# Optimization experiments

Measured on AMD Instinct MI355X. Metric: run time of the kernel, lower is better.

## Reference

```python
import jax, jax.numpy as jnp
import numpy as np

B, N, E, H = 4, 2048, 256, 8
D = E // H
EPS = 1e-5


def _layernorm(x, g, b):
    mu = jnp.mean(x, axis=-1, keepdims=True)
    var = jnp.mean(jnp.square(x - mu), axis=-1, keepdims=True)
    return (x - mu) * jax.lax.rsqrt(var + EPS) * g + b


def setup_inputs() -> dict:
    key = jax.random.key(0)
    ks = jax.random.split(key, 8)
    s = 1.0 / np.sqrt(E)
    lin = lambda k: (jax.random.normal(k, (E, E), jnp.float32) * s)
    return {
        "x_l": jax.random.normal(ks[0], (B, N, E), jnp.float32),
        "x_r": jax.random.normal(ks[1], (B, N, E), jnp.float32),
        "Wq": lin(ks[2]), "bq": jnp.zeros((E,), jnp.float32),
        "Wk": lin(ks[3]), "bk": jnp.zeros((E,), jnp.float32),
        "Wv": lin(ks[4]), "bv": jnp.zeros((E,), jnp.float32),
        "Wp": lin(ks[5]), "bp": jnp.zeros((E,), jnp.float32),
        "ln_g": jnp.ones((E,), jnp.float32), "ln_b": jnp.zeros((E,), jnp.float32),
        "rn_g": jnp.ones((E,), jnp.float32), "rn_b": jnp.zeros((E,), jnp.float32),
    }


def reference(x_l, x_r, Wq, bq, Wk, bk, Wv, bv, Wp, bp, ln_g, ln_b, rn_g, rn_b):
    # projections -> [b, h, n, d]
    q = (x_l @ Wq + bq).reshape(B, N, H, D).transpose(0, 2, 1, 3)
    k = (x_r @ Wk + bk).reshape(B, N, H, D).transpose(0, 2, 1, 3)
    # shared value from the difference of the two streams
    v = ((x_l - x_r) @ Wv + bv).reshape(B, N, H, D).transpose(0, 2, 1, 3)

    energy = jnp.einsum('bhqd,bhkd->bhqk', q, k)  # [b,h,n,n]
    attn = jax.nn.softmax(energy / np.sqrt(D), axis=-1)  # dropout p=0 (eval)

    # attn used as-is and transposed against the SAME value tensor
    out_l = jnp.einsum('bhqk,bhkd->bhqd', attn, v)
    out_r = jnp.einsum('bhqk,bhqd->bhkd', attn, v)  # == attn^T @ v

    out_l = out_l.transpose(0, 2, 1, 3).reshape(B, N, E)
    out_r = out_r.transpose(0, 2, 1, 3).reshape(B, N, E)

    out_l = _layernorm(out_l @ Wp + bp, ln_g, ln_b) + x_l
    out_r = _layernorm(out_r @ Wp + bp, rn_g, rn_b) + x_r
    return (out_l, out_r)
```

## Files before the change

### kernel.cpp

```cpp
#include <hip/hip_runtime.h>
#include <math.h>


typedef __attribute__((ext_vector_type(8))) short short8;
typedef __attribute__((ext_vector_type(4))) float f32x4;
typedef __attribute__((ext_vector_type(16))) float f32x16;
typedef __attribute__((ext_vector_type(4))) unsigned short u16x4;

union FragU { unsigned int u[4]; short8 s8; };

__device__ __forceinline__ unsigned short bf16_rn(float f) {
    union { float f; unsigned int u; } c; c.f = f;
    return (unsigned short)((c.u + 0x7FFFu + ((c.u >> 16) & 1u)) >> 16);
}
__device__ __forceinline__ float b2f(unsigned short u) {
    union { unsigned int i; float f; } c; c.i = ((unsigned int)u) << 16;
    return c.f;
}

#if __has_builtin(__builtin_amdgcn_exp2f)
__device__ __forceinline__ float fexp2(float x) { return __builtin_amdgcn_exp2f(x); }
#else
__device__ __forceinline__ float fexp2(float x) { return exp2f(x); }
#endif

__device__ __forceinline__ f32x4 mfma16(short8 a, short8 b, f32x4 c) {
    return __builtin_amdgcn_mfma_f32_16x16x32_bf16(a, b, c, 0, 0, 0);
}
__device__ __forceinline__ f32x16 mfma32(short8 a, short8 b, f32x16 c) {
    return __builtin_amdgcn_mfma_f32_32x32x16_bf16(a, b, c, 0, 0, 0);
}

__device__ __forceinline__ void plswap(unsigned int& x, unsigned int& y) {
    asm("v_permlane32_swap_b32 %0, %1" : "+v"(x), "+v"(y));
}

__device__ __forceinline__ short8 pfrag(unsigned int w0, unsigned int w1,
                                        unsigned int w2, unsigned int w3) {
    plswap(w0, w2);
    plswap(w1, w3);
    FragU fu;
    fu.u[0] = w0; fu.u[1] = w1; fu.u[2] = w2; fu.u[3] = w3;
    return fu.s8;
}

__global__ void prep_x(const float* __restrict__ xl, const float* __restrict__ xr,
                       unsigned short* __restrict__ xlb, unsigned short* __restrict__ xrb,
                       unsigned short* __restrict__ xdb) {
    const size_t i = ((size_t)blockIdx.x * 256 + threadIdx.x) * 4;
    const float4 A = *(const float4*)(xl + i);
    const float4 Bv = *(const float4*)(xr + i);
    u16x4 pa = { bf16_rn(A.x), bf16_rn(A.y), bf16_rn(A.z), bf16_rn(A.w) };
    u16x4 pb = { bf16_rn(Bv.x), bf16_rn(Bv.y), bf16_rn(Bv.z), bf16_rn(Bv.w) };
    u16x4 pd = { bf16_rn(A.x - Bv.x), bf16_rn(A.y - Bv.y),
                 bf16_rn(A.z - Bv.z), bf16_rn(A.w - Bv.w) };
    *(u16x4*)(xlb + i) = pa;
    *(u16x4*)(xrb + i) = pb;
    *(u16x4*)(xdb + i) = pd;
}

__global__ void prep_w(const float* __restrict__ Wq, const float* __restrict__ Wk,
                       const float* __restrict__ Wv, const float* __restrict__ Wp,
                       unsigned short* __restrict__ Wqt, unsigned short* __restrict__ Wkt,
                       unsigned short* __restrict__ Wvt, unsigned short* __restrict__ Wpt) {
    const int gid = blockIdx.x * 256 + threadIdx.x;
    const int m = gid >> 16;
    const int idx = gid & 65535;
    const int k = idx >> 8, n = idx & 255;
    const float* W = (m == 0) ? Wq : (m == 1) ? Wk : (m == 2) ? Wv : Wp;
    unsigned short* Wt = (m == 0) ? Wqt : (m == 1) ? Wkt : (m == 2) ? Wvt : Wpt;
    Wt[n * 256 + k] = bf16_rn(W[(size_t)k * 256 + n]);
}

__launch_bounds__(256)
__global__ void qkv_gemm(const unsigned short* __restrict__ xlb,
                         const unsigned short* __restrict__ xrb,
                         const unsigned short* __restrict__ xdb,
                         const unsigned short* __restrict__ Wqt,
                         const unsigned short* __restrict__ Wkt,
                         const unsigned short* __restrict__ Wvt,
                         const float* __restrict__ bq, const float* __restrict__ bk,
                         const float* __restrict__ bv,
                         unsigned short* __restrict__ Qg, unsigned short* __restrict__ Kg,
                         unsigned short* __restrict__ Vtg) {
    const int z = blockIdx.z;
    const unsigned short* A  = (z == 0) ? xlb : (z == 1) ? xrb : xdb;
    const unsigned short* Wt = (z == 0) ? Wqt : (z == 1) ? Wkt : Wvt;
    const float* bias        = (z == 0) ? bq  : (z == 1) ? bk  : bv;

    __shared__ unsigned short At[128][40];
    __shared__ unsigned short Bt[64][40];

    const int tid = threadIdx.x;
    const int lane = tid & 63, wv = tid >> 6;
    const int a = lane & 15, g = lane >> 4;
    const int wr = wv >> 1, wc = wv & 1;
    const int r0 = blockIdx.x * 128;
    const int c0 = blockIdx.y * 64;

    const f32x4 fz = {0.f, 0.f, 0.f, 0.f};
    f32x4 acc[4][2];
#pragma unroll
    for (int f = 0; f < 4; ++f)
#pragma unroll
        for (int t = 0; t < 2; ++t) acc[f][t] = fz;

    const int arow = tid >> 1, aoff = (tid & 1) * 16;
    const int brow = tid >> 2, boff = (tid & 3) * 8;

    for (int ks = 0; ks < 8; ++ks) {
        __syncthreads();
        {
            const unsigned short* asrc = A + (size_t)(r0 + arow) * 256 + ks * 32 + aoff;
            *(short8*)&At[arow][aoff]     = *(const short8*)asrc;
            *(short8*)&At[arow][aoff + 8] = *(const short8*)(asrc + 8);
            *(short8*)&Bt[brow][boff] =
                *(const short8*)(Wt + (size_t)(c0 + brow) * 256 + ks * 32 + boff);
        }
        __syncthreads();
        short8 af[4], bfr[2];
#pragma unroll
        for (int f = 0; f < 4; ++f) af[f] = *(const short8*)&At[wr * 64 + f * 16 + a][g * 8];
#pragma unroll
        for (int t = 0; t < 2; ++t) bfr[t] = *(const short8*)&Bt[wc * 32 + t * 16 + a][g * 8];
#pragma unroll
        for (int f = 0; f < 4; ++f)
#pragma unroll
            for (int t = 0; t < 2; ++t) acc[f][t] = mfma16(af[f], bfr[t], acc[f][t]);
    }

    const float scq = 0.17677669529663687f * 1.4426950408889634f;
#pragma unroll
    for (int t = 0; t < 2; ++t) {
        const int C = c0 + wc * 32 + t * 16 + a;
        const float bb = bias[C];
        const int h = C >> 5, d = C & 31;
#pragma unroll
        for (int f = 0; f < 4; ++f) {
            const int Rb = r0 + wr * 64 + f * 16 + g * 4;
            const int b_ = Rb >> 11, n = Rb & 2047;
            const int bhh = b_ * 8 + h;
            float v[4];
#pragma unroll
            for (int r = 0; r < 4; ++r) {
                v[r] = acc[f][t][r] + bb;
                if (z == 0) v[r] *= scq;
            }
            if (z < 2) {
                unsigned short* dst = ((z == 0) ? Qg : Kg) + (size_t)(bhh * 2048 + n) * 32 + d;
#pragma unroll
                for (int r = 0; r < 4; ++r) dst[(size_t)r * 32] = bf16_rn(v[r]);
            } else {
                u16x4 pk = { bf16_rn(v[0]), bf16_rn(v[1]), bf16_rn(v[2]), bf16_rn(v[3]) };
                *(u16x4*)(Vtg + (size_t)(bhh * 32 + d) * 2048 + n) = pk;
            }
        }
    }
}

#define P1_STEP(T, CUR)                                                         \
    {                                                                           \
        if ((T) < 31) *(short8*)((CUR) ? sd0 : sd1) = rr;                       \
        if ((T) < 30) rr = *(const short8*)(sgb + (size_t)(z * 32 + (T) + 2) * gstep); \
        const unsigned short* sb = (CUR) ? stz1 : stz0;                         \
        const short8 ck0 = *(const short8*)(sb + ro);                           \
        const short8 ck1 = *(const short8*)(sb + 512 + ro);                     \
        const short8 cv0 = *(const short8*)(sb + 1024 + ro);                    \
        const short8 cv1 = *(const short8*)(sb + 1536 + ro);                    \
        f32x16 s = {};                                                          \
        s = mfma32(ck0, qf0, s);                                                \
        s = mfma32(ck1, qf1, s);                                                \
        float p[16];                                                            \
        _Pragma("unroll") for (int j = 0; j < 16; ++j) p[j] = fexp2(s[j]);      \
        l_run += ((p[0] + p[1]) + (p[2] + p[3])) + ((p[4] + p[5]) + (p[6] + p[7])) \
               + ((p[8] + p[9]) + (p[10] + p[11])) + ((p[12] + p[13]) + (p[14] + p[15])); \
        unsigned int w[8];                                                      \
        _Pragma("unroll") for (int mm = 0; mm < 8; ++mm)                        \
            asm("v_cvt_pk_bf16_f32 %0, %1, %2"                                  \
                : "=v"(w[mm]) : "v"(p[2 * mm]), "v"(p[2 * mm + 1]));            \
        acc = mfma32(cv0, pfrag(w[0], w[1], w[2], w[3]), acc);                  \
        acc = mfma32(cv1, pfrag(w[4], w[5], w[6], w[7]), acc);                  \
        __syncthreads();                                                        \
    }

__launch_bounds__(512, 4)
__global__ void attn_pass1(const unsigned short* __restrict__ Qg,
                           const unsigned short* __restrict__ Kg,
                           const unsigned short* __restrict__ Vtg,
                           unsigned short* __restrict__ AOl,
                           unsigned short* __restrict__ Vsg) {
    __shared__ unsigned short ST[2][2][2][2][64][8];
    __shared__ float accS[4][16][64];
    __shared__ float lsumS[4][64];

    const int f = blockIdx.x;
    const int bh = 4 * (f & 7) + (f >> 7);
    const int qblk = (f >> 3) & 15;
    const int tid = threadIdx.x;
    const int wv = tid >> 6;
    const int qi = wv & 3, z = wv >> 2;
    const int lane = tid & 63, l31 = lane & 31, hi = lane >> 5;
    const int q0 = qblk * 128 + qi * 32;

    const unsigned short* Qb = Qg + (size_t)bh * 2048 * 32;
    const unsigned short* Kb = Kg + (size_t)bh * 2048 * 32;
    const unsigned short* Vb = Vtg + (size_t)bh * 32 * 2048;

    const short8 qf0 = *(const short8*)(Qb + (size_t)(q0 + l31) * 32 + hi * 8);
    const short8 qf1 = *(const short8*)(Qb + (size_t)(q0 + l31) * 32 + 16 + hi * 8);

    const int kv = qi >> 1;
    const int srow = (qi & 1) * 16 + (lane >> 2);
    const int m = lane & 3;
    unsigned short* sd0 = &ST[z][0][kv][m >> 1][srow + 32 * (m & 1)][0];
    unsigned short* sd1 = &ST[z][1][kv][m >> 1][srow + 32 * (m & 1)][0];
    const size_t gstep = kv ? 32 : 1024;
    const unsigned short* sgb = kv
        ? Vb + (size_t)srow * 2048 + m * 8
        : Kb + (size_t)srow * 32 + m * 8;

    const unsigned short* stz0 = &ST[z][0][0][0][0][0];
    const unsigned short* stz1 = &ST[z][1][0][0][0][0];
    const int ro = (l31 + 32 * hi) * 8;

    f32x16 acc = {};
    float l_run = 0.f;

    short8 rr = *(const short8*)(sgb + (size_t)(z * 32) * gstep);
    *(short8*)sd0 = rr;
    rr = *(const short8*)(sgb + (size_t)(z * 32 + 1) * gstep);
    __syncthreads();

    for (int tt = 0; tt < 16; ++tt) {
        P1_STEP(2 * tt, 0)
        P1_STEP(2 * tt + 1, 1)
    }

    float lsum = l_run + __shfl_xor(l_run, 32);

    if (z == 1) {
#pragma unroll
        for (int j = 0; j < 16; ++j) accS[qi][j][lane] = acc[j];
        lsumS[qi][lane] = lsum;
    }
    __syncthreads();
    if (z == 0) {
        lsum += lsumS[qi][lane];
        const float rl = 1.0f / lsum;
#pragma unroll
        for (int j = 0; j < 16; ++j) acc[j] += accS[qi][j][lane];

        const int b_ = bh >> 3, h = bh & 7;
        const int q = q0 + l31;
        unsigned short* dst = AOl + (size_t)(b_ * 2048 + q) * 256 + h * 32;
#pragma unroll
        for (int g2 = 0; g2 < 4; ++g2) {
            u16x4 pk = { bf16_rn(acc[4 * g2 + 0] * rl), bf16_rn(acc[4 * g2 + 1] * rl),
                         bf16_rn(acc[4 * g2 + 2] * rl), bf16_rn(acc[4 * g2 + 3] * rl) };
            *(u16x4*)(dst + 8 * g2 + 4 * hi) = pk;
        }
        if (hi == 0) lsumS[qi][l31] = rl;
    }
    __syncthreads();
    if (z == 1) {
        const int cb = hi * 16;
        float il[16];
#pragma unroll
        for (int e = 0; e < 16; e += 4) {
            const float4 v4 = *(const float4*)&lsumS[qi][cb + e];
            il[e] = v4.x; il[e + 1] = v4.y; il[e + 2] = v4.z; il[e + 3] = v4.w;
        }
        const unsigned short* vsrc = Vb + (size_t)l31 * 2048 + q0 + cb;
        unsigned short* vdst = Vsg + (size_t)bh * 32 * 2048 + (size_t)l31 * 2048 + q0 + cb;
#pragma unroll
        for (int c4 = 0; c4 < 4; ++c4) {
            const u16x4 vv = *(const u16x4*)(vsrc + c4 * 4);
            u16x4 o = { bf16_rn(b2f(vv.x) * il[c4 * 4 + 0]),
                        bf16_rn(b2f(vv.y) * il[c4 * 4 + 1]),
                        bf16_rn(b2f(vv.z) * il[c4 * 4 + 2]),
                        bf16_rn(b2f(vv.w) * il[c4 * 4 + 3]) };
            *(u16x4*)(vdst + c4 * 4) = o;
        }
    }
}

#define P2_STEP(T, CUR)                                                         \
    {                                                                           \
        if ((T) < 31) *(short8*)((CUR) ? sd0 : sd1) = rr;                       \
        if ((T) < 30) rr = *(const short8*)(sgb + (size_t)(z * 32 + (T) + 2) * gstep); \
        const unsigned short* sb = (CUR) ? stz1 : stz0;                         \
        const short8 cq0 = *(const short8*)(sb + ro);                           \
        const short8 cq1 = *(const short8*)(sb + 512 + ro);                     \
        const short8 cv0 = *(const short8*)(sb + 1024 + ro);                    \
        const short8 cv1 = *(const short8*)(sb + 1536 + ro);                    \
        f32x16 s = {};                                                          \
        s = mfma32(cq0, kf0, s);                                                \
        s = mfma32(cq1, kf1, s);                                                \
        float p[16];                                                            \
        _Pragma("unroll") for (int j = 0; j < 16; ++j) p[j] = fexp2(s[j]);      \
        unsigned int w[8];                                                      \
        _Pragma("unroll") for (int mm = 0; mm < 8; ++mm)                        \
            asm("v_cvt_pk_bf16_f32 %0, %1, %2"                                  \
                : "=v"(w[mm]) : "v"(p[2 * mm]), "v"(p[2 * mm + 1]));            \
        acc = mfma32(pfrag(w[0], w[1], w[2], w[3]), cv0, acc);                  \
        acc = mfma32(pfrag(w[4], w[5], w[6], w[7]), cv1, acc);                  \
        __syncthreads();                                                        \
    }

__launch_bounds__(512, 4)
__global__ void attn_pass2(const unsigned short* __restrict__ Qg,
                           const unsigned short* __restrict__ Kg,
                           const unsigned short* __restrict__ Vsg,
                           unsigned short* __restrict__ AOr) {
    __shared__ unsigned short ST[2][2][2][2][64][8];
    __shared__ float accS[4][16][64];

    const int f = blockIdx.x;
    const int bh = 4 * (f & 7) + (f >> 7);
    const int kblk = (f >> 3) & 15;
    const int tid = threadIdx.x;
    const int wv = tid >> 6;
    const int ki = wv & 3, z = wv >> 2;
    const int lane = tid & 63, l31 = lane & 31, hi = lane >> 5;
    const int k0 = kblk * 128 + ki * 32;

    const unsigned short* Qb = Qg + (size_t)bh * 2048 * 32;
    const unsigned short* Kb = Kg + (size_t)bh * 2048 * 32;
    const unsigned short* Vb = Vsg + (size_t)bh * 32 * 2048;

    const short8 kf0 = *(const short8*)(Kb + (size_t)(k0 + l31) * 32 + hi * 8);
    const short8 kf1 = *(const short8*)(Kb + (size_t)(k0 + l31) * 32 + 16 + hi * 8);

    const int kv = ki >> 1;
    const int srow = (ki & 1) * 16 + (lane >> 2);
    const int m = lane & 3;
    unsigned short* sd0 = &ST[z][0][kv][m >> 1][srow + 32 * (m & 1)][0];
    unsigned short* sd1 = &ST[z][1][kv][m >> 1][srow + 32 * (m & 1)][0];
    const size_t gstep = kv ? 32 : 1024;
    const unsigned short* sgb = kv
        ? Vb + (size_t)srow * 2048 + m * 8
        : Qb + (size_t)srow * 32 + m * 8;

    const unsigned short* stz0 = &ST[z][0][0][0][0][0];
    const unsigned short* stz1 = &ST[z][1][0][0][0][0];
    const int ro = (l31 + 32 * hi) * 8;

    f32x16 acc = {};

    short8 rr = *(const short8*)(sgb + (size_t)(z * 32) * gstep);
    *(short8*)sd0 = rr;
    rr = *(const short8*)(sgb + (size_t)(z * 32 + 1) * gstep);
    __syncthreads();

    for (int tt = 0; tt < 16; ++tt) {
        P2_STEP(2 * tt, 0)
        P2_STEP(2 * tt + 1, 1)
    }

    if (z == 1) {
#pragma unroll
        for (int j = 0; j < 16; ++j) accS[ki][j][lane] = acc[j];
    }
    __syncthreads();
    if (z == 0) {
#pragma unroll
        for (int j = 0; j < 16; ++j) acc[j] += accS[ki][j][lane];

        const int b_ = bh >> 3, h = bh & 7;
#pragma unroll
        for (int j = 0; j < 16; ++j) {
            const int krow = k0 + (j & 3) + 8 * (j >> 2) + 4 * hi;
            AOr[(size_t)(b_ * 2048 + krow) * 256 + h * 32 + l31] = bf16_rn(acc[j]);
        }
    }
}

__launch_bounds__(256)
__global__ void proj_ln(const unsigned short* __restrict__ AO,
                        const unsigned short* __restrict__ Wpt,
                        const float* __restrict__ bp,
                        const float* __restrict__ gamma, const float* __restrict__ beta,
                        const float* __restrict__ xres,
                        float* __restrict__ out) {
    __shared__ unsigned short At[64][264];
    __shared__ unsigned short Bt[256][40];

    const int tid = threadIdx.x;
    const int lane = tid & 63, wv = tid >> 6;
    const int a = lane & 15, g = lane >> 4;
    const int r0 = blockIdx.x * 64;

    {
        const int row = tid >> 2, seg = (tid & 3) * 64;
        const unsigned short* src = AO + (size_t)(r0 + row) * 256 + seg;
#pragma unroll
        for (int i = 0; i < 8; ++i)
            *(short8*)&At[row][seg + i * 8] = *(const short8*)(src + i * 8);
    }

    const f32x4 fz = {0.f, 0.f, 0.f, 0.f};
    f32x4 acc[16];
#pragma unroll
    for (int cf = 0; cf < 16; ++cf) acc[cf] = fz;

    for (int ks = 0; ks < 8; ++ks) {
        __syncthreads();
        {
            const unsigned short* src = Wpt + (size_t)tid * 256 + ks * 32;
#pragma unroll
            for (int i = 0; i < 4; ++i)
                *(short8*)&Bt[tid][i * 8] = *(const short8*)(src + i * 8);
        }
        __syncthreads();
        const short8 af = *(const short8*)&At[wv * 16 + a][ks * 32 + g * 8];
#pragma unroll
        for (int cf = 0; cf < 16; ++cf) {
            const short8 bfr = *(const short8*)&Bt[cf * 16 + a][g * 8];
            acc[cf] = mfma16(af, bfr, acc[cf]);
        }
    }

    float bb[16], gg[16], be[16];
#pragma unroll
    for (int cf = 0; cf < 16; ++cf) {
        const int c = cf * 16 + a;
        bb[cf] = bp[c]; gg[cf] = gamma[c]; be[cf] = beta[c];
    }
#pragma unroll
    for (int r = 0; r < 4; ++r) {
        float y[16];
        float s1 = 0.f, s2 = 0.f;
#pragma unroll
        for (int cf = 0; cf < 16; ++cf) {
            y[cf] = acc[cf][r] + bb[cf];
            s1 += y[cf];
            s2 += y[cf] * y[cf];
        }
#pragma unroll
        for (int mask = 1; mask <= 8; mask <<= 1) {
            s1 += __shfl_xor(s1, mask);
            s2 += __shfl_xor(s2, mask);
        }
        const float mu = s1 * (1.0f / 256.0f);
        const float var = s2 * (1.0f / 256.0f) - mu * mu;
        const float rstd = rsqrtf(var + 1e-5f);
        const int R = r0 + wv * 16 + g * 4 + r;
#pragma unroll
        for (int cf = 0; cf < 16; ++cf) {
            const int c = cf * 16 + a;
            out[(size_t)R * 256 + c] =
                (y[cf] - mu) * rstd * gg[cf] + be[cf] + xres[(size_t)R * 256 + c];
        }
    }
}

extern "C" void kernel_launch(void* const* d_in, const int* in_sizes, int n_in,
                              void* d_out, int out_size, void* d_ws, size_t ws_size,
                              hipStream_t stream) {
    const float* x_l  = (const float*)d_in[0];
    const float* x_r  = (const float*)d_in[1];
    const float* Wq   = (const float*)d_in[2];
    const float* bq   = (const float*)d_in[3];
    const float* Wk   = (const float*)d_in[4];
    const float* bk   = (const float*)d_in[5];
    const float* Wv   = (const float*)d_in[6];
    const float* bv   = (const float*)d_in[7];
    const float* Wp   = (const float*)d_in[8];
    const float* bp   = (const float*)d_in[9];
    const float* ln_g = (const float*)d_in[10];
    const float* ln_b = (const float*)d_in[11];
    const float* rn_g = (const float*)d_in[12];
    const float* rn_b = (const float*)d_in[13];

    const size_t SZ_TOK = (size_t)8192 * 256;

    unsigned short* xl_bf = (unsigned short*)d_ws;
    unsigned short* xr_bf = xl_bf + SZ_TOK;
    unsigned short* xd_bf = xr_bf + SZ_TOK;
    unsigned short* Qg    = xd_bf + SZ_TOK;
    unsigned short* Kg    = Qg + SZ_TOK;
    unsigned short* Vtg   = Kg + SZ_TOK;
    unsigned short* Wqt   = Vtg + SZ_TOK;
    unsigned short* Wkt   = Wqt + 65536;
    unsigned short* Wvt   = Wkt + 65536;
    unsigned short* Wpt   = Wvt + 65536;
    unsigned short* AOl   = xl_bf;
    unsigned short* AOr   = xr_bf;
    unsigned short* Vs    = xd_bf;
    float* out = (float*)d_out;

    prep_x<<<2048, 256, 0, stream>>>(x_l, x_r, xl_bf, xr_bf, xd_bf);
    prep_w<<<1024, 256, 0, stream>>>(Wq, Wk, Wv, Wp, Wqt, Wkt, Wvt, Wpt);
    qkv_gemm<<<dim3(64, 4, 3), 256, 0, stream>>>(xl_bf, xr_bf, xd_bf,
                                                 Wqt, Wkt, Wvt, bq, bk, bv, Qg, Kg, Vtg);
    attn_pass1<<<512, 512, 0, stream>>>(Qg, Kg, Vtg, AOl, Vs);
    attn_pass2<<<512, 512, 0, stream>>>(Qg, Kg, Vs, AOr);
    proj_ln<<<128, 256, 0, stream>>>(AOl, Wpt, bp, ln_g, ln_b, x_l, out);
    proj_ln<<<128, 256, 0, stream>>>(AOr, Wpt, bp, rn_g, rn_b, x_r, out + SZ_TOK);
}
```

Baseline: 104.2 us.

## Double-buffer GEMM and attention tiles, merge prep and proj launches

Merges the prep_x and prep_w kernels into one launch, and the two proj_ln launches into one grid that uses blockIdx.y to pick the stream. Adds LDS double-buffering in qkv_gemm and proj_ln so the next K-slice is staged while the current one is consumed, leaving one barrier per step. The attention passes now stage two KV tiles per phase and sync once per pair instead of once per tile. The aim is fewer launches and less barrier stall, at the cost of more shared memory, which may lower occupancy in the 4-blocks-per-CU attention kernels.

Result: faster. 90.37 us (-13.3%).

```diff
diff --git a/kernel.cpp b/kernel.cpp
--- a/kernel.cpp
+++ b/kernel.cpp
@@ -44,32 +44,34 @@
     return fu.s8;
 }
 
-__global__ void prep_x(const float* __restrict__ xl, const float* __restrict__ xr,
-                       unsigned short* __restrict__ xlb, unsigned short* __restrict__ xrb,
-                       unsigned short* __restrict__ xdb) {
-    const size_t i = ((size_t)blockIdx.x * 256 + threadIdx.x) * 4;
-    const float4 A = *(const float4*)(xl + i);
-    const float4 Bv = *(const float4*)(xr + i);
-    u16x4 pa = { bf16_rn(A.x), bf16_rn(A.y), bf16_rn(A.z), bf16_rn(A.w) };
-    u16x4 pb = { bf16_rn(Bv.x), bf16_rn(Bv.y), bf16_rn(Bv.z), bf16_rn(Bv.w) };
-    u16x4 pd = { bf16_rn(A.x - Bv.x), bf16_rn(A.y - Bv.y),
-                 bf16_rn(A.z - Bv.z), bf16_rn(A.w - Bv.w) };
-    *(u16x4*)(xlb + i) = pa;
-    *(u16x4*)(xrb + i) = pb;
-    *(u16x4*)(xdb + i) = pd;
-}
-
-__global__ void prep_w(const float* __restrict__ Wq, const float* __restrict__ Wk,
-                       const float* __restrict__ Wv, const float* __restrict__ Wp,
-                       unsigned short* __restrict__ Wqt, unsigned short* __restrict__ Wkt,
-                       unsigned short* __restrict__ Wvt, unsigned short* __restrict__ Wpt) {
-    const int gid = blockIdx.x * 256 + threadIdx.x;
-    const int m = gid >> 16;
-    const int idx = gid & 65535;
-    const int k = idx >> 8, n = idx & 255;
-    const float* W = (m == 0) ? Wq : (m == 1) ? Wk : (m == 2) ? Wv : Wp;
-    unsigned short* Wt = (m == 0) ? Wqt : (m == 1) ? Wkt : (m == 2) ? Wvt : Wpt;
-    Wt[n * 256 + k] = bf16_rn(W[(size_t)k * 256 + n]);
+__global__ void prep_all(const float* __restrict__ xl, const float* __restrict__ xr,
+                         const float* __restrict__ Wq, const float* __restrict__ Wk,
+                         const float* __restrict__ Wv, const float* __restrict__ Wp,
+                         unsigned short* __restrict__ xlb, unsigned short* __restrict__ xrb,
+                         unsigned short* __restrict__ xdb,
+                         unsigned short* __restrict__ Wqt, unsigned short* __restrict__ Wkt,
+                         unsigned short* __restrict__ Wvt, unsigned short* __restrict__ Wpt) {
+    const int bid = blockIdx.x;
+    if (bid < 2048) {
+        const size_t i = ((size_t)bid * 256 + threadIdx.x) * 4;
+        const float4 A = *(const float4*)(xl + i);
+        const float4 Bv = *(const float4*)(xr + i);
+        u16x4 pa = { bf16_rn(A.x), bf16_rn(A.y), bf16_rn(A.z), bf16_rn(A.w) };
+        u16x4 pb = { bf16_rn(Bv.x), bf16_rn(Bv.y), bf16_rn(Bv.z), bf16_rn(Bv.w) };
+        u16x4 pd = { bf16_rn(A.x - Bv.x), bf16_rn(A.y - Bv.y),
+                     bf16_rn(A.z - Bv.z), bf16_rn(A.w - Bv.w) };
+        *(u16x4*)(xlb + i) = pa;
+        *(u16x4*)(xrb + i) = pb;
+        *(u16x4*)(xdb + i) = pd;
+    } else {
+        const int gid = (bid - 2048) * 256 + threadIdx.x;
+        const int m = gid >> 16;
+        const int idx = gid & 65535;
+        const int k = idx >> 8, n = idx & 255;
+        const float* W = (m == 0) ? Wq : (m == 1) ? Wk : (m == 2) ? Wv : Wp;
+        unsigned short* Wt = (m == 0) ? Wqt : (m == 1) ? Wkt : (m == 2) ? Wvt : Wpt;
+        Wt[n * 256 + k] = bf16_rn(W[(size_t)k * 256 + n]);
+    }
 }
 
 __launch_bounds__(256)
@@ -88,8 +90,8 @@
     const unsigned short* Wt = (z == 0) ? Wqt : (z == 1) ? Wkt : Wvt;
     const float* bias        = (z == 0) ? bq  : (z == 1) ? bk  : bv;
 
-    __shared__ unsigned short At[128][40];
-    __shared__ unsigned short Bt[64][40];
+    __shared__ unsigned short At[2][128][40];
+    __shared__ unsigned short Bt[2][64][40];
 
     const int tid = threadIdx.x;
     const int lane = tid & 63, wv = tid >> 6;
@@ -107,27 +109,35 @@
 
     const int arow = tid >> 1, aoff = (tid & 1) * 16;
     const int brow = tid >> 2, boff = (tid & 3) * 8;
-
+    const unsigned short* asrc = A + (size_t)(r0 + arow) * 256 + aoff;
+    const unsigned short* bsrc = Wt + (size_t)(c0 + brow) * 256 + boff;
+
+#define QKV_STAGE(KS, BUF)                                                      \
+    {                                                                           \
+        *(short8*)&At[BUF][arow][aoff]     = *(const short8*)(asrc + (KS) * 32); \
+        *(short8*)&At[BUF][arow][aoff + 8] = *(const short8*)(asrc + (KS) * 32 + 8); \
+        *(short8*)&Bt[BUF][brow][boff]     = *(const short8*)(bsrc + (KS) * 32); \
+    }
+
+    QKV_STAGE(0, 0)
+    __syncthreads();
+
+#pragma unroll
     for (int ks = 0; ks < 8; ++ks) {
+        const int b = ks & 1;
+        if (ks < 7) QKV_STAGE(ks + 1, b ^ 1)
+        short8 af[4], bfr[2];
+#pragma unroll
+        for (int f = 0; f < 4; ++f) af[f] = *(const short8*)&At[b][wr * 64 + f * 16 + a][g * 8];
+#pragma unroll
+        for (int t = 0; t < 2; ++t) bfr[t] = *(const short8*)&Bt[b][wc * 32 + t * 16 + a][g * 8];
+#pragma unroll
+        for (int f = 0; f < 4; ++f)
+#pragma unroll
+            for (int t = 0; t < 2; ++t) acc[f][t] = mfma16(af[f], bfr[t], acc[f][t]);
         __syncthreads();
-        {
-            const unsigned short* asrc = A + (size_t)(r0 + arow) * 256 + ks * 32 + aoff;
-            *(short8*)&At[arow][aoff]     = *(const short8*)asrc;
-            *(short8*)&At[arow][aoff + 8] = *(const short8*)(asrc + 8);
-            *(short8*)&Bt[brow][boff] =
-                *(const short8*)(Wt + (size_t)(c0 + brow) * 256 + ks * 32 + boff);
-        }
-        __syncthreads();
-        short8 af[4], bfr[2];
-#pragma unroll
-        for (int f = 0; f < 4; ++f) af[f] = *(const short8*)&At[wr * 64 + f * 16 + a][g * 8];
-#pragma unroll
-        for (int t = 0; t < 2; ++t) bfr[t] = *(const short8*)&Bt[wc * 32 + t * 16 + a][g * 8];
-#pragma unroll
-        for (int f = 0; f < 4; ++f)
-#pragma unroll
-            for (int t = 0; t < 2; ++t) acc[f][t] = mfma16(af[f], bfr[t], acc[f][t]);
-    }
+    }
+#undef QKV_STAGE
 
     const float scq = 0.17677669529663687f * 1.4426950408889634f;
 #pragma unroll
@@ -158,29 +168,25 @@
     }
 }
 
-#define P1_STEP(T, CUR)                                                         \
+#define P1_TILE(SB)                                                             \
     {                                                                           \
-        if ((T) < 31) *(short8*)((CUR) ? sd0 : sd1) = rr;                       \
-        if ((T) < 30) rr = *(const short8*)(sgb + (size_t)(z * 32 + (T) + 2) * gstep); \
-        const unsigned short* sb = (CUR) ? stz1 : stz0;                         \
-        const short8 ck0 = *(const short8*)(sb + ro);                           \
-        const short8 ck1 = *(const short8*)(sb + 512 + ro);                     \
-        const short8 cv0 = *(const short8*)(sb + 1024 + ro);                    \
-        const short8 cv1 = *(const short8*)(sb + 1536 + ro);                    \
+        const short8 ck0 = *(const short8*)((SB) + ro);                         \
+        const short8 ck1 = *(const short8*)((SB) + 512 + ro);                   \
+        const short8 cv0 = *(const short8*)((SB) + 1024 + ro);                  \
+        const short8 cv1 = *(const short8*)((SB) + 1536 + ro);                  \
         f32x16 s = {};                                                          \
         s = mfma32(ck0, qf0, s);                                                \
         s = mfma32(ck1, qf1, s);                                                \
         float p[16];                                                            \
         _Pragma("unroll") for (int j = 0; j < 16; ++j) p[j] = fexp2(s[j]);      \
-        l_run += ((p[0] + p[1]) + (p[2] + p[3])) + ((p[4] + p[5]) + (p[6] + p[7])) \
-               + ((p[8] + p[9]) + (p[10] + p[11])) + ((p[12] + p[13]) + (p[14] + p[15])); \
+        l_run += (((p[0] + p[1]) + (p[2] + p[3])) + ((p[4] + p[5]) + (p[6] + p[7]))) \
+               + (((p[8] + p[9]) + (p[10] + p[11])) + ((p[12] + p[13]) + (p[14] + p[15]))); \
         unsigned int w[8];                                                      \
         _Pragma("unroll") for (int mm = 0; mm < 8; ++mm)                        \
             asm("v_cvt_pk_bf16_f32 %0, %1, %2"                                  \
                 : "=v"(w[mm]) : "v"(p[2 * mm]), "v"(p[2 * mm + 1]));            \
         acc = mfma32(cv0, pfrag(w[0], w[1], w[2], w[3]), acc);                  \
         acc = mfma32(cv1, pfrag(w[4], w[5], w[6], w[7]), acc);                  \
-        __syncthreads();                                                        \
     }
 
 __launch_bounds__(512, 4)
@@ -189,7 +195,7 @@
                            const unsigned short* __restrict__ Vtg,
                            unsigned short* __restrict__ AOl,
                            unsigned short* __restrict__ Vsg) {
-    __shared__ unsigned short ST[2][2][2][2][64][8];
+    __shared__ unsigned short ST[2][2][2][2][2][64][8];
     __shared__ float accS[4][16][64];
     __shared__ float lsumS[4][64];
 
@@ -212,28 +218,48 @@
     const int kv = qi >> 1;
     const int srow = (qi & 1) * 16 + (lane >> 2);
     const int m = lane & 3;
-    unsigned short* sd0 = &ST[z][0][kv][m >> 1][srow + 32 * (m & 1)][0];
-    unsigned short* sd1 = &ST[z][1][kv][m >> 1][srow + 32 * (m & 1)][0];
+    unsigned short* wp00 = &ST[z][0][0][kv][m >> 1][srow + 32 * (m & 1)][0];
+    unsigned short* wp01 = &ST[z][0][1][kv][m >> 1][srow + 32 * (m & 1)][0];
+    unsigned short* wp10 = &ST[z][1][0][kv][m >> 1][srow + 32 * (m & 1)][0];
+    unsigned short* wp11 = &ST[z][1][1][kv][m >> 1][srow + 32 * (m & 1)][0];
     const size_t gstep = kv ? 32 : 1024;
     const unsigned short* sgb = kv
         ? Vb + (size_t)srow * 2048 + m * 8
         : Kb + (size_t)srow * 32 + m * 8;
-
-    const unsigned short* stz0 = &ST[z][0][0][0][0][0];
-    const unsigned short* stz1 = &ST[z][1][0][0][0][0];
+    const int zt = z * 32;
+
+    const unsigned short* rb00 = &ST[z][0][0][0][0][0][0];
+    const unsigned short* rb01 = &ST[z][0][1][0][0][0][0];
+    const unsigned short* rb10 = &ST[z][1][0][0][0][0][0];
+    const unsigned short* rb11 = &ST[z][1][1][0][0][0][0];
     const int ro = (l31 + 32 * hi) * 8;
 
     f32x16 acc = {};
     float l_run = 0.f;
 
-    short8 rr = *(const short8*)(sgb + (size_t)(z * 32) * gstep);
-    *(short8*)sd0 = rr;
-    rr = *(const short8*)(sgb + (size_t)(z * 32 + 1) * gstep);
-    __syncthreads();
-
-    for (int tt = 0; tt < 16; ++tt) {
-        P1_STEP(2 * tt, 0)
-        P1_STEP(2 * tt + 1, 1)
+    short8 rr0 = *(const short8*)(sgb + (size_t)(zt + 0) * gstep);
+    short8 rr1 = *(const short8*)(sgb + (size_t)(zt + 1) * gstep);
+    *(short8*)wp00 = rr0;
+    *(short8*)wp01 = rr1;
+    rr0 = *(const short8*)(sgb + (size_t)(zt + 2) * gstep);
+    rr1 = *(const short8*)(sgb + (size_t)(zt + 3) * gstep);
+    __syncthreads();
+
+#pragma unroll
+    for (int ph = 0; ph < 16; ++ph) {
+        const int pb = ph & 1;
+        unsigned short* wA = pb ? wp00 : wp10;
+        unsigned short* wB = pb ? wp01 : wp11;
+        const unsigned short* rA = pb ? rb10 : rb00;
+        const unsigned short* rB = pb ? rb11 : rb01;
+        if (ph < 15) { *(short8*)wA = rr0; *(short8*)wB = rr1; }
+        if (ph < 14) {
+            rr0 = *(const short8*)(sgb + (size_t)(zt + 2 * ph + 4) * gstep);
+            rr1 = *(const short8*)(sgb + (size_t)(zt + 2 * ph + 5) * gstep);
+        }
+        P1_TILE(rA)
+        P1_TILE(rB)
+        __syncthreads();
     }
 
     float lsum = l_run + __shfl_xor(l_run, 32);
@@ -284,15 +310,12 @@
     }
 }
 
-#define P2_STEP(T, CUR)                                                         \
+#define P2_TILE(SB)                                                             \
     {                                                                           \
-        if ((T) < 31) *(short8*)((CUR) ? sd0 : sd1) = rr;                       \
-        if ((T) < 30) rr = *(const short8*)(sgb + (size_t)(z * 32 + (T) + 2) * gstep); \
-        const unsigned short* sb = (CUR) ? stz1 : stz0;                         \
-        const short8 cq0 = *(const short8*)(sb + ro);                           \
-        const short8 cq1 = *(const short8*)(sb + 512 + ro);                     \
-        const short8 cv0 = *(const short8*)(sb + 1024 + ro);                    \
-        const short8 cv1 = *(const short8*)(sb + 1536 + ro);                    \
+        const short8 cq0 = *(const short8*)((SB) + ro);                         \
+        const short8 cq1 = *(const short8*)((SB) + 512 + ro);                   \
+        const short8 cv0 = *(const short8*)((SB) + 1024 + ro);                  \
+        const short8 cv1 = *(const short8*)((SB) + 1536 + ro);                  \
         f32x16 s = {};                                                          \
         s = mfma32(cq0, kf0, s);                                                \
         s = mfma32(cq1, kf1, s);                                                \
@@ -304,7 +327,6 @@
                 : "=v"(w[mm]) : "v"(p[2 * mm]), "v"(p[2 * mm + 1]));            \
         acc = mfma32(pfrag(w[0], w[1], w[2], w[3]), cv0, acc);                  \
         acc = mfma32(pfrag(w[4], w[5], w[6], w[7]), cv1, acc);                  \
-        __syncthreads();                                                        \
     }
 
 __launch_bounds__(512, 4)
@@ -312,7 +334,7 @@
                            const unsigned short* __restrict__ Kg,
                            const unsigned short* __restrict__ Vsg,
                            unsigned short* __restrict__ AOr) {
-    __shared__ unsigned short ST[2][2][2][2][64][8];
+    __shared__ unsigned short ST[2][2][2][2][2][64][8];
     __shared__ float accS[4][16][64];
 
     const int f = blockIdx.x;
@@ -334,27 +356,47 @@
     const int kv = ki >> 1;
     const int srow = (ki & 1) * 16 + (lane >> 2);
     const int m = lane & 3;
-    unsigned short* sd0 = &ST[z][0][kv][m >> 1][srow + 32 * (m & 1)][0];
-    unsigned short* sd1 = &ST[z][1][kv][m >> 1][srow + 32 * (m & 1)][0];
+    unsigned short* wp00 = &ST[z][0][0][kv][m >> 1][srow + 32 * (m & 1)][0];
+    unsigned short* wp01 = &ST[z][0][1][kv][m >> 1][srow + 32 * (m & 1)][0];
+    unsigned short* wp10 = &ST[z][1][0][kv][m >> 1][srow + 32 * (m & 1)][0];
+    unsigned short* wp11 = &ST[z][1][1][kv][m >> 1][srow + 32 * (m & 1)][0];
     const size_t gstep = kv ? 32 : 1024;
     const unsigned short* sgb = kv
         ? Vb + (size_t)srow * 2048 + m * 8
         : Qb + (size_t)srow * 32 + m * 8;
-
-    const unsigned short* stz0 = &ST[z][0][0][0][0][0];
-    const unsigned short* stz1 = &ST[z][1][0][0][0][0];
+    const int zt = z * 32;
+
+    const unsigned short* rb00 = &ST[z][0][0][0][0][0][0];
+    const unsigned short* rb01 = &ST[z][0][1][0][0][0][0];
+    const unsigned short* rb10 = &ST[z][1][0][0][0][0][0];
+    const unsigned short* rb11 = &ST[z][1][1][0][0][0][0];
     const int ro = (l31 + 32 * hi) * 8;
 
     f32x16 acc = {};
 
-    short8 rr = *(const short8*)(sgb + (size_t)(z * 32) * gstep);
-    *(short8*)sd0 = rr;
-    rr = *(const short8*)(sgb + (size_t)(z * 32 + 1) * gstep);
-    __syncthreads();
-
-    for (int tt = 0; tt < 16; ++tt) {
-        P2_STEP(2 * tt, 0)
-        P2_STEP(2 * tt + 1, 1)
+    short8 rr0 = *(const short8*)(sgb + (size_t)(zt + 0) * gstep);
+    short8 rr1 = *(const short8*)(sgb + (size_t)(zt + 1) * gstep);
+    *(short8*)wp00 = rr0;
+    *(short8*)wp01 = rr1;
+    rr0 = *(const short8*)(sgb + (size_t)(zt + 2) * gstep);
+    rr1 = *(const short8*)(sgb + (size_t)(zt + 3) * gstep);
+    __syncthreads();
+
+#pragma unroll
+    for (int ph = 0; ph < 16; ++ph) {
+        const int pb = ph & 1;
+        unsigned short* wA = pb ? wp00 : wp10;
+        unsigned short* wB = pb ? wp01 : wp11;
+        const unsigned short* rA = pb ? rb10 : rb00;
+        const unsigned short* rB = pb ? rb11 : rb01;
+        if (ph < 15) { *(short8*)wA = rr0; *(short8*)wB = rr1; }
+        if (ph < 14) {
+            rr0 = *(const short8*)(sgb + (size_t)(zt + 2 * ph + 4) * gstep);
+            rr1 = *(const short8*)(sgb + (size_t)(zt + 2 * ph + 5) * gstep);
+        }
+        P2_TILE(rA)
+        P2_TILE(rB)
+        __syncthreads();
     }
 
     if (z == 1) {
@@ -376,14 +418,23 @@
 }
 
 __launch_bounds__(256)
-__global__ void proj_ln(const unsigned short* __restrict__ AO,
+__global__ void proj_ln(const unsigned short* __restrict__ AOl,
+                        const unsigned short* __restrict__ AOr,
                         const unsigned short* __restrict__ Wpt,
                         const float* __restrict__ bp,
-                        const float* __restrict__ gamma, const float* __restrict__ beta,
-                        const float* __restrict__ xres,
+                        const float* __restrict__ ln_g, const float* __restrict__ ln_b,
+                        const float* __restrict__ rn_g, const float* __restrict__ rn_b,
+                        const float* __restrict__ xl, const float* __restrict__ xr,
                         float* __restrict__ out) {
     __shared__ unsigned short At[64][264];
-    __shared__ unsigned short Bt[256][40];
+    __shared__ unsigned short Bt[2][256][40];
+
+    const int sel = blockIdx.y;
+    const unsigned short* AO = sel ? AOr : AOl;
+    const float* gamma = sel ? rn_g : ln_g;
+    const float* beta  = sel ? rn_b : ln_b;
+    const float* xres  = sel ? xr : xl;
+    float* o = out + (size_t)sel * 8192 * 256;
 
     const int tid = threadIdx.x;
     const int lane = tid & 63, wv = tid >> 6;
@@ -397,27 +448,36 @@
         for (int i = 0; i < 8; ++i)
             *(short8*)&At[row][seg + i * 8] = *(const short8*)(src + i * 8);
     }
+    const unsigned short* wsrc = Wpt + (size_t)tid * 256;
+    {
+#pragma unroll
+        for (int i = 0; i < 4; ++i)
+            *(short8*)&Bt[0][tid][i * 8] = *(const short8*)(wsrc + i * 8);
+    }
 
     const f32x4 fz = {0.f, 0.f, 0.f, 0.f};
     f32x4 acc[16];
 #pragma unroll
     for (int cf = 0; cf < 16; ++cf) acc[cf] = fz;
 
+    __syncthreads();
+
+#pragma unroll
     for (int ks = 0; ks < 8; ++ks) {
+        const int b = ks & 1;
+        if (ks < 7) {
+#pragma unroll
+            for (int i = 0; i < 4; ++i)
+                *(short8*)&Bt[b ^ 1][tid][i * 8] =
+                    *(const short8*)(wsrc + (ks + 1) * 32 + i * 8);
+        }
+        const short8 af = *(const short8*)&At[wv * 16 + a][ks * 32 + g * 8];
+#pragma unroll
+        for (int cf = 0; cf < 16; ++cf) {
+            const short8 bfr = *(const short8*)&Bt[b][cf * 16 + a][g * 8];
+            acc[cf] = mfma16(af, bfr, acc[cf]);
+        }
         __syncthreads();
-        {
-            const unsigned short* src = Wpt + (size_t)tid * 256 + ks * 32;
-#pragma unroll
-            for (int i = 0; i < 4; ++i)
-                *(short8*)&Bt[tid][i * 8] = *(const short8*)(src + i * 8);
-        }
-        __syncthreads();
-        const short8 af = *(const short8*)&At[wv * 16 + a][ks * 32 + g * 8];
-#pragma unroll
-        for (int cf = 0; cf < 16; ++cf) {
-            const short8 bfr = *(const short8*)&Bt[cf * 16 + a][g * 8];
-            acc[cf] = mfma16(af, bfr, acc[cf]);
-        }
     }
 
     float bb[16], gg[16], be[16];
@@ -448,7 +508,7 @@
 #pragma unroll
         for (int cf = 0; cf < 16; ++cf) {
             const int c = cf * 16 + a;
-            out[(size_t)R * 256 + c] =
+            o[(size_t)R * 256 + c] =
                 (y[cf] - mu) * rstd * gg[cf] + be[cf] + xres[(size_t)R * 256 + c];
         }
     }
@@ -489,12 +549,12 @@
     unsigned short* Vs    = xd_bf;
     float* out = (float*)d_out;
 
-    prep_x<<<2048, 256, 0, stream>>>(x_l, x_r, xl_bf, xr_bf, xd_bf);
-    prep_w<<<1024, 256, 0, stream>>>(Wq, Wk, Wv, Wp, Wqt, Wkt, Wvt, Wpt);
+    prep_all<<<3072, 256, 0, stream>>>(x_l, x_r, Wq, Wk, Wv, Wp,
+                                       xl_bf, xr_bf, xd_bf, Wqt, Wkt, Wvt, Wpt);
     qkv_gemm<<<dim3(64, 4, 3), 256, 0, stream>>>(xl_bf, xr_bf, xd_bf,
                                                  Wqt, Wkt, Wvt, bq, bk, bv, Qg, Kg, Vtg);
     attn_pass1<<<512, 512, 0, stream>>>(Qg, Kg, Vtg, AOl, Vs);
     attn_pass2<<<512, 512, 0, stream>>>(Qg, Kg, Vs, AOr);
-    proj_ln<<<128, 256, 0, stream>>>(AOl, Wpt, bp, ln_g, ln_b, x_l, out);
-    proj_ln<<<128, 256, 0, stream>>>(AOr, Wpt, bp, rn_g, rn_b, x_r, out + SZ_TOK);
-}
+    proj_ln<<<dim3(128, 2), 256, 0, stream>>>(AOl, AOr, Wpt, bp,
+                                              ln_g, ln_b, rn_g, rn_b, x_l, x_r, out);
+}
```
